# Kernel optimization log

Measured on AMD Instinct MI355X. Metric: run time of the kernel, lower is better.

Reference implementation:

```python
import jax, jax.numpy as jnp
import numpy as np

DIM = 768
NUM_HEADS = 12
HEAD_DIM = DIM // NUM_HEADS
SCALE = HEAD_DIM ** -0.5
EPS = 1e-6


def setup_inputs() -> dict:
    key = jax.random.key(0)
    k_x, k_p, k_qkv, k_proj = jax.random.split(key, 4)
    B, N = 16, 577
    x = jax.random.normal(k_x, (B, N, DIM), dtype=jnp.float32)
    # binary keep/drop policy per token (as produced by an upstream gumbel gate)
    policy = jax.random.randint(k_p, (B, N, 1), 0, 2).astype(jnp.float32)
    Wqkv = jax.random.normal(k_qkv, (DIM, 3 * DIM), dtype=jnp.float32) * 0.02
    bqkv = jnp.zeros((3 * DIM,), dtype=jnp.float32)
    Wproj = jax.random.normal(k_proj, (DIM, DIM), dtype=jnp.float32) * 0.02
    bproj = jnp.zeros((DIM,), dtype=jnp.float32)
    return {"x": x, "policy": policy, "Wqkv": Wqkv, "bqkv": bqkv,
            "Wproj": Wproj, "bproj": bproj}


def reference(x, policy, Wqkv, bqkv, Wproj, bproj):
    B, N, C = x.shape
    # qkv projection -> [3, B, H, N, Dh]
    qkv = (x @ Wqkv + bqkv).reshape(B, N, 3, NUM_HEADS, HEAD_DIM)
    qkv = jnp.transpose(qkv, (2, 0, 3, 1, 4))
    q, k, v = qkv[0], qkv[1], qkv[2]
    # scaled attention logits [B, H, N, N]
    attn = jnp.einsum("bhnd,bhmd->bhnm", q, k) * SCALE
    # policy-masked softmax (training-mode formula: eye keeps self-attention alive)
    ap = policy.reshape(B, 1, 1, N)
    eye = jnp.eye(N, dtype=ap.dtype).reshape(1, 1, N, N)
    ap = ap + (1.0 - ap) * eye
    max_att = jnp.max(attn, axis=-1, keepdims=True)
    e = jnp.exp(attn - max_att) * ap
    attn = (e + EPS / N) / (jnp.sum(e, axis=-1, keepdims=True) + EPS)
    # attend and project
    out = jnp.einsum("bhnm,bhmd->bhnd", attn, v)
    out = jnp.transpose(out, (0, 2, 1, 3)).reshape(B, N, C)
    return out @ Wproj + bproj
```

## Files before the change

kernel.cpp:

```cpp
#include <hip/hip_runtime.h>
#include <hip/hip_bf16.h>

#define QKVC   2304
#define NHEAD  12
#define NTOK   577
#define NBATCH 16
#define NROWS  (NBATCH * NTOK)
#define NPAD   640
#define SCALE  0.125f
#define EPSV   1e-6f
#define KT     24
#define CH     512

typedef __bf16  bf16x8 __attribute__((ext_vector_type(8)));
typedef float   f32x4  __attribute__((ext_vector_type(4)));

__device__ __forceinline__ unsigned short f2bf(float f) {
    union { float f; unsigned u; } v; v.f = f;
    unsigned r = v.u + 0x7FFFu + ((v.u >> 16) & 1u);
    return (unsigned short)(r >> 16);
}
__device__ __forceinline__ unsigned short f2bf_trunc(float f) {
    return (unsigned short)(__float_as_uint(f) >> 16);
}
__device__ __forceinline__ unsigned pack2bf(float a, float b) {
    return (unsigned)f2bf(a) | ((unsigned)f2bf(b) << 16);
}
__device__ __forceinline__ f32x4 mfma16(bf16x8 a, bf16x8 b, f32x4 c) {
    return __builtin_amdgcn_mfma_f32_16x16x32_bf16(a, b, c, 0, 0, 0);
}

#define GLDS16(g, l) __builtin_amdgcn_global_load_lds( \
    (const __attribute__((address_space(1))) unsigned int*)(g), \
    (__attribute__((address_space(3))) unsigned int*)(l), 16, 0, 0)


__device__ void transpose_tile(const float* __restrict__ src, unsigned short* __restrict__ dst,
                               int N, int bx, int by, int t) {
    __shared__ unsigned short lt[64 * 72];
    int n0 = bx * 64, k0 = by * 64;
    int kk = t >> 4, nn = (t & 15) * 4;
    for (int i = 0; i < 4; i++) {
        int kr = kk + i * 16;
        float4 v = *(const float4*)&src[(size_t)(k0 + kr) * N + n0 + nn];
        lt[(nn + 0) * 72 + kr] = f2bf(v.x);
        lt[(nn + 1) * 72 + kr] = f2bf(v.y);
        lt[(nn + 2) * 72 + kr] = f2bf(v.z);
        lt[(nn + 3) * 72 + kr] = f2bf(v.w);
    }
    __syncthreads();
    int n = t >> 2;
    int ks = (t & 3) * 16;
    int gn = n0 + n;
    int ntile = gn >> 4, r = gn & 15, s = (r >> 1) & 3;
    for (int j = 0; j < 2; j++) {
        int k = k0 + ks + j * 8;
        int kt = k >> 5;
        int q = ((k >> 3) & 3) ^ s;
        uint4 v = *(uint4*)&lt[n * 72 + ks + j * 8];
        *(uint4*)&dst[((size_t)ntile * KT + kt) * CH + r * 32 + q * 8] = v;
    }
}

#define NCHUNK (577 * KT)
#define CONVB  ((NCHUNK + 15) / 16)
__global__ void k_prep(const float* __restrict__ x, unsigned short* __restrict__ xbt,
                       const float* __restrict__ Wqkv, unsigned short* __restrict__ wqkvt,
                       const float* __restrict__ Wproj, unsigned short* __restrict__ wprojt) {
    int id = blockIdx.x, t = threadIdx.x;
    if (id < CONVB) {
        int cid = id * 16 + (t >> 4);
        if (cid < NCHUNK) {
            int r = t & 15;
            int mt = cid / KT, kt = cid - mt * KT;
            const float* src = x + ((size_t)mt * 16 + r) * 768 + kt * 32;
            int s = (r >> 1) & 3;
            unsigned short* dst = xbt + (size_t)cid * CH + r * 32;
            #pragma unroll
            for (int q = 0; q < 4; q++) {
                int g = q ^ s;
                float4 v0 = *(const float4*)(src + g * 8);
                float4 v1 = *(const float4*)(src + g * 8 + 4);
                uint4 u;
                u.x = pack2bf(v0.x, v0.y);
                u.y = pack2bf(v0.z, v0.w);
                u.z = pack2bf(v1.x, v1.y);
                u.w = pack2bf(v1.z, v1.w);
                *(uint4*)(dst + q * 8) = u;
            }
        }
    } else if (id < CONVB + 432) {
        int i2 = id - CONVB;
        transpose_tile(Wqkv, wqkvt, QKVC, i2 % 36, i2 / 36, t);
    } else {
        int i2 = id - CONVB - 432;
        transpose_tile(Wproj, wprojt, 768, i2 % 12, i2 / 12, t);
    }
}

template <bool F32OUT>
__global__ __launch_bounds__(512, 2)
void k_gemm(const unsigned short* __restrict__ A, const unsigned short* __restrict__ B,
            const float* __restrict__ bias, void* __restrict__ outp, int Ncols,
            unsigned short* __restrict__ vt) {
    __shared__ unsigned short SL[36864];
    int t = threadIdx.x;
    int lane = t & 63, wave = t >> 6, quad = lane >> 4, l15 = lane & 15;
    int wm = wave >> 2, wn = wave & 3;
    int nT = Ncols >> 7;
    int nwg = gridDim.x;

    int q8 = nwg >> 3, r8 = nwg & 7;
    int xcd = blockIdx.x & 7, idx = blockIdx.x >> 3;
    int wg = (xcd < r8 ? xcd * (q8 + 1) : r8 * (q8 + 1) + (xcd - r8) * q8) + idx;
    int m0 = (wg / nT) * 256;
    int n0 = (wg % nT) * 128;

    const unsigned short* gA0 = A + ((size_t)((m0 >> 4) + wave) * KT) * CH + lane * 8;
    const unsigned short* gA1 = gA0 + (size_t)8 * KT * CH;
    const unsigned short* gB0 = B + ((size_t)((n0 >> 4) + wave) * KT) * CH + lane * 8;

    f32x4 acc[8][2] = {};

    auto STAGE = [&](int sx, unsigned slot) {
        unsigned sa = slot * 8192u + (unsigned)wave * 512u;
        unsigned sb = 24576u + slot * 4096u + (unsigned)wave * 512u;
        GLDS16(gA0 + sx * CH, &SL[sa]);
        GLDS16(gA1 + sx * CH, &SL[sa + 4096]);
        GLDS16(gB0 + sx * CH, &SL[sb]);
    };

    auto STEP = [&](unsigned slot, int sx, unsigned sslot, bool stage) {
        unsigned ab = slot * 8192u;
        unsigned bb = 24576u + slot * 4096u;
        unsigned ro = (unsigned)(quad ^ ((l15 >> 1) & 3)) * 8u;
        bf16x8 af[8], bfr[2];
        #pragma unroll
        for (int i = 0; i < 8; i++)
            af[i]  = *(const bf16x8*)&SL[ab + (unsigned)(wm * 128 + i * 16 + l15) * 32u + ro];
        #pragma unroll
        for (int i = 0; i < 2; i++)
            bfr[i] = *(const bf16x8*)&SL[bb + (unsigned)(wn * 32 + i * 16 + l15) * 32u + ro];
        if (stage) STAGE(sx, sslot);
        asm volatile("s_waitcnt lgkmcnt(0)" ::: "memory");
        __builtin_amdgcn_s_setprio(1);
        #pragma unroll
        for (int mi = 0; mi < 8; mi++)
            #pragma unroll
            for (int ni = 0; ni < 2; ni++)
                acc[mi][ni] = mfma16(af[mi], bfr[ni], acc[mi][ni]);
        __builtin_amdgcn_s_setprio(0);
    };

    STAGE(0, 0); STAGE(1, 1);
    for (int s = 0; s < 23; s++) {
        asm volatile("s_waitcnt vmcnt(3)" ::: "memory");
        asm volatile("s_barrier" ::: "memory");
        STEP((unsigned)(s % 3), s + 2, (unsigned)((s + 2) % 3), s < 22);
    }
    asm volatile("s_waitcnt vmcnt(0)" ::: "memory");
    asm volatile("s_barrier" ::: "memory");
    STEP(2u, 0, 0u, false);

    if constexpr (F32OUT) {
        for (int ni = 0; ni < 2; ni++) {
            int col = n0 + wn * 32 + ni * 16 + l15;
            float bv = bias[col];
            for (int mi = 0; mi < 8; mi++) {
                int rowm = m0 + wm * 128 + mi * 16 + quad * 4;
                for (int r = 0; r < 4; r++) {
                    int m = rowm + r;
                    if (m < NROWS)
                        ((float*)outp)[(size_t)m * Ncols + col] = acc[mi][ni][r] + bv;
                }
            }
        }
    } else {
        __syncthreads();
        for (int ni = 0; ni < 2; ni++) {
            int colL = wn * 32 + ni * 16 + l15;
            float bv = bias[n0 + colL];
            for (int mi = 0; mi < 8; mi++) {
                int rowL = wm * 128 + mi * 16 + quad * 4;
                for (int r = 0; r < 4; r++)
                    SL[(rowL + r) * 136 + colL] = f2bf(acc[mi][ni][r] + bv);
            }
        }
        __syncthreads();
        if (n0 < 1536) {
            for (int rr = 0; rr < 8; rr++) {
                int row = rr * 32 + (t >> 4);
                int m = m0 + row;
                if (m < NROWS) {
                    uint4 v = *(uint4*)&SL[row * 136 + (t & 15) * 8];
                    *(uint4*)&((unsigned short*)outp)[(size_t)m * Ncols + n0 + (t & 15) * 8] = v;
                }
            }
        } else {
            int h0 = (n0 - 1536) >> 6;
            for (int i = 0; i < 16; i++) {
                int c = wave * 16 + i;
                int h = h0 + (c >> 6), d = c & 63;
                for (int half = 0; half < 4; half++) {
                    int lr = half * 64 + lane;
                    int m = m0 + lr;
                    if (m < NROWS) {
                        unsigned bbx = (unsigned)m / 577u;
                        int tok = m - (int)bbx * 577;
                        vt[(((size_t)bbx * NHEAD + h) * 64 + d) * NPAD + tok] =
                            SL[lr * 136 + c];
                    }
                }
            }
        }
    }
}

__global__ __launch_bounds__(256, 4)
void k_attn(const unsigned short* __restrict__ qkv, const unsigned short* __restrict__ vt,
            const float* __restrict__ policy, unsigned short* __restrict__ ao) {
    __shared__ unsigned short Ks[64 * 72];
    __shared__ unsigned short Vs[64 * 72];
    __shared__ unsigned short Ps[4][32 * 72];
    __shared__ float pol[NPAD];
    int t = threadIdx.x;
    int lane = t & 63, wave = t >> 6, quad = lane >> 4, l15 = lane & 15;
    int b = blockIdx.z, h = blockIdx.y, qt = blockIdx.x;
    const unsigned short* qbase = qkv + (size_t)(b * NTOK) * QKVC + h * 64;
    const unsigned short* kbase = qkv + (size_t)(b * NTOK) * QKVC + 768 + h * 64;
    const unsigned short* vbase = vt + (size_t)(b * NHEAD + h) * 64 * NPAD;

    for (int i = t; i < NPAD; i += 256)
        pol[i] = (i < NTOK) ? policy[b * NTOK + i] : 0.f;

    bf16x8 qf[2][2];
    for (int mi = 0; mi < 2; mi++) {
        const unsigned short* qp =
            qbase + (size_t)(qt * 128 + mi * 64 + wave * 16 + l15) * QKVC + quad * 8;
        qf[mi][0] = *(const bf16x8*)qp;
        qf[mi][1] = *(const bf16x8*)(qp + 32);
    }
    bf16x8 onesf;
    for (int j = 0; j < 8; j++) onesf[j] = (__bf16)1.0f;
    f32x4 o[2][4] = {};
    f32x4 ls[2] = {};
    int rowtok0[2];
    for (int mi = 0; mi < 2; mi++)
        rowtok0[mi] = qt * 128 + mi * 64 + wave * 16 + quad * 4;
    __syncthreads();

    for (int kt = 0; kt < 10; kt++) {
        int key0 = kt * 64;
        for (int i = t; i < 512; i += 256) {
            int row = i >> 3, seg = (i & 7) * 8;
            *(uint4*)&Ks[row * 72 + seg] = *(const uint4*)&kbase[(size_t)(key0 + row) * QKVC + seg];
            *(uint4*)&Vs[row * 72 + seg] = *(const uint4*)&vbase[(size_t)row * NPAD + key0 + seg];
        }
        __syncthreads();

        for (int ci = 0; ci < 4; ci++) {
            bf16x8 kf0 = *(const bf16x8*)&Ks[(ci * 16 + l15) * 72 + quad * 8];
            bf16x8 kf1 = *(const bf16x8*)&Ks[(ci * 16 + l15) * 72 + 32 + quad * 8];
            int col = key0 + ci * 16 + l15;
            float pc = pol[col];
            for (int mi = 0; mi < 2; mi++) {
                f32x4 a = {};
                a = mfma16(qf[mi][0], kf0, a);
                a = mfma16(qf[mi][1], kf1, a);
                for (int r = 0; r < 4; r++) {
                    float ap = (col == rowtok0[mi] + r) ? 1.f : pc;
                    float e = __expf(a[r] * SCALE) * ap;
                    Ps[wave][(mi * 16 + quad * 4 + r) * 72 + ci * 16 + l15] = f2bf_trunc(e);
                }
            }
        }
        __asm__ volatile("s_waitcnt lgkmcnt(0)" ::: "memory");
        bf16x8 pf[2][2];
        for (int mi = 0; mi < 2; mi++) {
            pf[mi][0] = *(const bf16x8*)&Ps[wave][(mi * 16 + l15) * 72 + quad * 8];
            pf[mi][1] = *(const bf16x8*)&Ps[wave][(mi * 16 + l15) * 72 + 32 + quad * 8];
            ls[mi] = mfma16(pf[mi][0], onesf, ls[mi]);
            ls[mi] = mfma16(pf[mi][1], onesf, ls[mi]);
        }
        for (int di = 0; di < 4; di++) {
            bf16x8 vf0 = *(const bf16x8*)&Vs[(di * 16 + l15) * 72 + quad * 8];
            bf16x8 vf1 = *(const bf16x8*)&Vs[(di * 16 + l15) * 72 + 32 + quad * 8];
            for (int mi = 0; mi < 2; mi++) {
                o[mi][di] = mfma16(pf[mi][0], vf0, o[mi][di]);
                o[mi][di] = mfma16(pf[mi][1], vf1, o[mi][di]);
            }
        }
        __syncthreads();
    }

    for (int mi = 0; mi < 2; mi++) {
        for (int r = 0; r < 4; r++) {
            int tok = rowtok0[mi] + r;
            if (tok < NTOK) {
                float inv = __builtin_amdgcn_rcpf(ls[mi][r] + EPSV);
                int m = b * NTOK + tok;
                int mt = m >> 4, rr = m & 15, s = (rr >> 1) & 3;
                unsigned short* dst = ao + ((size_t)mt * KT) * CH + rr * 32;
                for (int di = 0; di < 4; di++) {
                    int k = h * 64 + di * 16 + l15;
                    int kt2 = k >> 5;
                    int q = ((k >> 3) & 3) ^ s;
                    dst[(size_t)kt2 * CH + q * 8 + (l15 & 7)] =
                        f2bf(o[mi][di][r] * inv);
                }
            }
        }
    }
}

extern "C" void kernel_launch(void* const* d_in, const int* in_sizes, int n_in,
                              void* d_out, int out_size, void* d_ws, size_t ws_size,
                              hipStream_t stream) {
    const float* x      = (const float*)d_in[0];
    const float* policy = (const float*)d_in[1];
    const float* Wqkv   = (const float*)d_in[2];
    const float* bqkv   = (const float*)d_in[3];
    const float* Wproj  = (const float*)d_in[4];
    const float* bproj  = (const float*)d_in[5];
    float* out = (float*)d_out;

    unsigned short* p = (unsigned short*)d_ws;
    unsigned short* xb     = p;
    unsigned short* ao     = p; p += (size_t)NROWS * 768;
    unsigned short* wqkvt  = p; p += (size_t)QKVC * 768;
    unsigned short* wprojt = p; p += (size_t)768 * 768;
    unsigned short* qkvb   = p; p += (size_t)NROWS * QKVC;
    unsigned short* vt     = p; p += (size_t)NBATCH * NHEAD * 64 * NPAD;

    int mT = (NROWS + 255) / 256;

    k_prep<<<CONVB + 432 + 144, 256, 0, stream>>>(x, xb, Wqkv, wqkvt, Wproj, wprojt);
    k_gemm<false><<<mT * (QKVC / 128), 512, 0, stream>>>(
        xb, wqkvt, bqkv, (void*)qkvb, QKVC, vt);
    k_attn<<<dim3(NPAD / 128, NHEAD, NBATCH), 256, 0, stream>>>(qkvb, vt, policy, ao);
    k_gemm<true><<<mT * (768 / 128), 512, 0, stream>>>(
        ao, wprojt, bproj, (void*)out, 768, nullptr);
}
```

Measured before the change: 191.0 us.

## Store K/V in pre-swizzled MFMA tiles and double-buffer attention loads

The QKV GEMM epilogue now writes K and V per (batch, head) into padded, XOR-swizzled 16x32 tile layouts, and Q into its own compact buffer. The attention kernel stages K/V tiles into double-buffered LDS with direct global-to-LDS loads, so the next tile's load overlaps the current tile's compute. Work-groups are remapped by XCD, the exp is computed with exp2 on a prescaled constant, and occupancy drops to 3 because LDS use is larger. The padded K/V tails are zeroed in the prep kernel.

```diff
diff --git a/kernel.cpp b/kernel.cpp
--- a/kernel.cpp
+++ b/kernel.cpp
@@ -11,6 +11,7 @@
 #define EPSV   1e-6f
 #define KT     24
 #define CH     512
+#define EXPC   0.18033688011f
 
 typedef __bf16  bf16x8 __attribute__((ext_vector_type(8)));
 typedef float   f32x4  __attribute__((ext_vector_type(4)));
@@ -66,7 +67,8 @@
 #define CONVB  ((NCHUNK + 15) / 16)
 __global__ void k_prep(const float* __restrict__ x, unsigned short* __restrict__ xbt,
                        const float* __restrict__ Wqkv, unsigned short* __restrict__ wqkvt,
-                       const float* __restrict__ Wproj, unsigned short* __restrict__ wprojt) {
+                       const float* __restrict__ Wproj, unsigned short* __restrict__ wprojt,
+                       unsigned short* __restrict__ ktc, unsigned short* __restrict__ vtc) {
     int id = blockIdx.x, t = threadIdx.x;
     if (id < CONVB) {
         int cid = id * 16 + (t >> 4);
@@ -92,9 +94,17 @@
     } else if (id < CONVB + 432) {
         int i2 = id - CONVB;
         transpose_tile(Wqkv, wqkvt, QKVC, i2 % 36, i2 / 36, t);
-    } else {
+    } else if (id < CONVB + 432 + 144) {
         int i2 = id - CONVB - 432;
         transpose_tile(Wproj, wprojt, 768, i2 % 12, i2 / 12, t);
+    } else {
+        int bh = id - CONVB - 576;
+        size_t base = (size_t)bh * 40960 + 36864;
+        uint4 z = {0u, 0u, 0u, 0u};
+        for (int i = t; i < 512; i += 256) {
+            *(uint4*)&ktc[base + (size_t)i * 8] = z;
+            *(uint4*)&vtc[base + (size_t)i * 8] = z;
+        }
     }
 }
 
@@ -102,7 +112,7 @@
 __global__ __launch_bounds__(512, 2)
 void k_gemm(const unsigned short* __restrict__ A, const unsigned short* __restrict__ B,
             const float* __restrict__ bias, void* __restrict__ outp, int Ncols,
-            unsigned short* __restrict__ vt) {
+            unsigned short* __restrict__ ktp, unsigned short* __restrict__ vtp) {
     __shared__ unsigned short SL[36864];
     int t = threadIdx.x;
     int lane = t & 63, wave = t >> 6, quad = lane >> 4, l15 = lane & 15;
@@ -187,13 +197,30 @@
             }
         }
         __syncthreads();
-        if (n0 < 1536) {
+        if (n0 < 768) {
             for (int rr = 0; rr < 8; rr++) {
                 int row = rr * 32 + (t >> 4);
                 int m = m0 + row;
                 if (m < NROWS) {
                     uint4 v = *(uint4*)&SL[row * 136 + (t & 15) * 8];
-                    *(uint4*)&((unsigned short*)outp)[(size_t)m * Ncols + n0 + (t & 15) * 8] = v;
+                    *(uint4*)&((unsigned short*)outp)[(size_t)m * 768 + n0 + (t & 15) * 8] = v;
+                }
+            }
+        } else if (n0 < 1536) {
+            int cseg = (t & 15) * 8;
+            int h = ((n0 - 768) >> 6) + (cseg >> 6);
+            int d = cseg & 63;
+            int dh = d >> 5, q = (d >> 3) & 3;
+            for (int rr = 0; rr < 8; rr++) {
+                int row = rr * 32 + (t >> 4);
+                int m = m0 + row;
+                if (m < NROWS) {
+                    unsigned bbx = (unsigned)m / 577u;
+                    int tok = m - (int)bbx * 577;
+                    int r16 = tok & 15, s = (r16 >> 1) & 3;
+                    uint4 v = *(uint4*)&SL[row * 136 + cseg];
+                    *(uint4*)&ktp[((((size_t)bbx * NHEAD + h) * 40 + (tok >> 4)) * 2 + dh) * 512
+                                  + r16 * 32 + (q ^ s) * 8] = v;
                 }
             }
         } else {
@@ -201,14 +228,17 @@
             for (int i = 0; i < 16; i++) {
                 int c = wave * 16 + i;
                 int h = h0 + (c >> 6), d = c & 63;
+                int dt = d >> 4, r = d & 15, sr = (r >> 1) & 3;
                 for (int half = 0; half < 4; half++) {
                     int lr = half * 64 + lane;
                     int m = m0 + lr;
                     if (m < NROWS) {
                         unsigned bbx = (unsigned)m / 577u;
                         int tok = m - (int)bbx * 577;
-                        vt[(((size_t)bbx * NHEAD + h) * 64 + d) * NPAD + tok] =
-                            SL[lr * 136 + c];
+                        int tb = tok >> 6, kh = (tok >> 5) & 1, k32 = tok & 31;
+                        int q = ((k32 >> 3) & 3) ^ sr;
+                        vtp[((((size_t)bbx * NHEAD + h) * 10 + tb) * 8 + dt * 2 + kh) * 512
+                            + r * 32 + q * 8 + (k32 & 7)] = SL[lr * 136 + c];
                     }
                 }
             }
@@ -216,19 +246,22 @@
     }
 }
 
-__global__ __launch_bounds__(256, 4)
-void k_attn(const unsigned short* __restrict__ qkv, const unsigned short* __restrict__ vt,
+__global__ __launch_bounds__(256, 3)
+void k_attn(const unsigned short* __restrict__ Qb, const unsigned short* __restrict__ ktc,
+            const unsigned short* __restrict__ vtc,
             const float* __restrict__ policy, unsigned short* __restrict__ ao) {
-    __shared__ unsigned short Ks[64 * 72];
-    __shared__ unsigned short Vs[64 * 72];
+    __shared__ unsigned short Kb[2][4096];
+    __shared__ unsigned short Vb[2][4096];
     __shared__ unsigned short Ps[4][32 * 72];
     __shared__ float pol[NPAD];
     int t = threadIdx.x;
     int lane = t & 63, wave = t >> 6, quad = lane >> 4, l15 = lane & 15;
-    int b = blockIdx.z, h = blockIdx.y, qt = blockIdx.x;
-    const unsigned short* qbase = qkv + (size_t)(b * NTOK) * QKVC + h * 64;
-    const unsigned short* kbase = qkv + (size_t)(b * NTOK) * QKVC + 768 + h * 64;
-    const unsigned short* vbase = vt + (size_t)(b * NHEAD + h) * 64 * NPAD;
+    int wg = (blockIdx.x & 7) * 120 + (blockIdx.x >> 3);
+    int qt = wg % 5, bh = wg / 5;
+    int h = bh % NHEAD, b = bh / NHEAD;
+    const unsigned short* qbase = Qb + (size_t)(b * NTOK) * 768 + h * 64;
+    const unsigned short* kcb = ktc + (size_t)bh * 40960 + lane * 8;
+    const unsigned short* vcb = vtc + (size_t)bh * 40960 + lane * 8;
 
     for (int i = t; i < NPAD; i += 256)
         pol[i] = (i < NTOK) ? policy[b * NTOK + i] : 0.f;
@@ -236,7 +269,7 @@
     bf16x8 qf[2][2];
     for (int mi = 0; mi < 2; mi++) {
         const unsigned short* qp =
-            qbase + (size_t)(qt * 128 + mi * 64 + wave * 16 + l15) * QKVC + quad * 8;
+            qbase + (size_t)(qt * 128 + mi * 64 + wave * 16 + l15) * 768 + quad * 8;
         qf[mi][0] = *(const bf16x8*)qp;
         qf[mi][1] = *(const bf16x8*)(qp + 32);
     }
@@ -247,20 +280,32 @@
     int rowtok0[2];
     for (int mi = 0; mi < 2; mi++)
         rowtok0[mi] = qt * 128 + mi * 64 + wave * 16 + quad * 4;
+
+    auto STAGEA = [&](int kt) {
+        int buf = kt & 1;
+        GLDS16(kcb + ((size_t)(kt * 4 + wave) * 2 + 0) * 512, &Kb[buf][(wave * 2 + 0) * 512]);
+        GLDS16(kcb + ((size_t)(kt * 4 + wave) * 2 + 1) * 512, &Kb[buf][(wave * 2 + 1) * 512]);
+        GLDS16(vcb + ((size_t)(kt * 8 + wave * 2 + 0)) * 512, &Vb[buf][(wave * 2 + 0) * 512]);
+        GLDS16(vcb + ((size_t)(kt * 8 + wave * 2 + 1)) * 512, &Vb[buf][(wave * 2 + 1) * 512]);
+    };
+
+    STAGEA(0);
     __syncthreads();
 
     for (int kt = 0; kt < 10; kt++) {
+        if (kt) {
+            asm volatile("s_waitcnt vmcnt(0)" ::: "memory");
+            asm volatile("s_barrier" ::: "memory");
+        }
+        if (kt < 9) STAGEA(kt + 1);
+        const unsigned short* KB = &Kb[kt & 1][0];
+        const unsigned short* VB = &Vb[kt & 1][0];
+        unsigned ro = (unsigned)(quad ^ ((l15 >> 1) & 3)) * 8u;
         int key0 = kt * 64;
-        for (int i = t; i < 512; i += 256) {
-            int row = i >> 3, seg = (i & 7) * 8;
-            *(uint4*)&Ks[row * 72 + seg] = *(const uint4*)&kbase[(size_t)(key0 + row) * QKVC + seg];
-            *(uint4*)&Vs[row * 72 + seg] = *(const uint4*)&vbase[(size_t)row * NPAD + key0 + seg];
-        }
-        __syncthreads();
 
         for (int ci = 0; ci < 4; ci++) {
-            bf16x8 kf0 = *(const bf16x8*)&Ks[(ci * 16 + l15) * 72 + quad * 8];
-            bf16x8 kf1 = *(const bf16x8*)&Ks[(ci * 16 + l15) * 72 + 32 + quad * 8];
+            bf16x8 kf0 = *(const bf16x8*)&KB[(ci * 2 + 0) * 512 + l15 * 32 + ro];
+            bf16x8 kf1 = *(const bf16x8*)&KB[(ci * 2 + 1) * 512 + l15 * 32 + ro];
             int col = key0 + ci * 16 + l15;
             float pc = pol[col];
             for (int mi = 0; mi < 2; mi++) {
@@ -269,7 +314,7 @@
                 a = mfma16(qf[mi][1], kf1, a);
                 for (int r = 0; r < 4; r++) {
                     float ap = (col == rowtok0[mi] + r) ? 1.f : pc;
-                    float e = __expf(a[r] * SCALE) * ap;
+                    float e = __builtin_amdgcn_exp2f(a[r] * EXPC) * ap;
                     Ps[wave][(mi * 16 + quad * 4 + r) * 72 + ci * 16 + l15] = f2bf_trunc(e);
                 }
             }
@@ -283,14 +328,13 @@
             ls[mi] = mfma16(pf[mi][1], onesf, ls[mi]);
         }
         for (int di = 0; di < 4; di++) {
-            bf16x8 vf0 = *(const bf16x8*)&Vs[(di * 16 + l15) * 72 + quad * 8];
-            bf16x8 vf1 = *(const bf16x8*)&Vs[(di * 16 + l15) * 72 + 32 + quad * 8];
+            bf16x8 vf0 = *(const bf16x8*)&VB[(di * 2 + 0) * 512 + l15 * 32 + ro];
+            bf16x8 vf1 = *(const bf16x8*)&VB[(di * 2 + 1) * 512 + l15 * 32 + ro];
             for (int mi = 0; mi < 2; mi++) {
                 o[mi][di] = mfma16(pf[mi][0], vf0, o[mi][di]);
                 o[mi][di] = mfma16(pf[mi][1], vf1, o[mi][di]);
             }
         }
-        __syncthreads();
     }
 
     for (int mi = 0; mi < 2; mi++) {
@@ -329,15 +373,18 @@
     unsigned short* ao     = p; p += (size_t)NROWS * 768;
     unsigned short* wqkvt  = p; p += (size_t)QKVC * 768;
     unsigned short* wprojt = p; p += (size_t)768 * 768;
-    unsigned short* qkvb   = p; p += (size_t)NROWS * QKVC;
-    unsigned short* vt     = p; p += (size_t)NBATCH * NHEAD * 64 * NPAD;
+    unsigned short* Qb     = p; p += (size_t)NROWS * 768;
+    unsigned short* ktc    = p; p += (size_t)NBATCH * NHEAD * 40960;
+    unsigned short* vtc    = p; p += (size_t)NBATCH * NHEAD * 40960;
 
     int mT = (NROWS + 255) / 256;
 
-    k_prep<<<CONVB + 432 + 144, 256, 0, stream>>>(x, xb, Wqkv, wqkvt, Wproj, wprojt);
+    k_prep<<<CONVB + 432 + 144 + 192, 256, 0, stream>>>(
+        x, xb, Wqkv, wqkvt, Wproj, wprojt, ktc, vtc);
     k_gemm<false><<<mT * (QKVC / 128), 512, 0, stream>>>(
-        xb, wqkvt, bqkv, (void*)qkvb, QKVC, vt);
-    k_attn<<<dim3(NPAD / 128, NHEAD, NBATCH), 256, 0, stream>>>(qkvb, vt, policy, ao);
+        xb, wqkvt, bqkv, (void*)Qb, QKVC, ktc, vtc);
+    k_attn<<<NPAD / 128 * NHEAD * NBATCH, 256, 0, stream>>>(
+        Qb, ktc, vtc, policy, ao);
     k_gemm<true><<<mT * (768 / 128), 512, 0, stream>>>(
-        ao, wprojt, bproj, (void*)out, 768, nullptr);
-}
+        ao, wprojt, bproj, (void*)out, 768, nullptr, nullptr);
+}
```

Result: no change. 193.0 us (+1.0%).
